# Kernel tuning notes

Hardware: AMD Instinct MI355X
Metric: run time of the kernel (lower is better)

Reference implementation:

```python
import jax, jax.numpy as jnp
import numpy as np

IMG = 640
TOPK = 13
NC = 1
ALPHA = 0.5
BETA = 6.0
EPS = 1e-9
IOU_EPS = 1e-7


def _make_anchors():
    pts = []
    for s in (8, 16, 32):
        n = IMG // s
        g = (jnp.arange(n, dtype=jnp.float32) + 0.5) * s
        yy, xx = jnp.meshgrid(g, g, indexing="ij")
        pts.append(jnp.stack([xx.ravel(), yy.ravel()], axis=-1))
    return jnp.concatenate(pts, axis=0)  # [8400, 2]


def _make_boxes(key, prefix):
    k1, k2 = jax.random.split(key)
    cxcy = jax.random.uniform(k1, prefix + (2,), minval=32.0, maxval=IMG - 32.0)
    wh = jax.random.uniform(k2, prefix + (2,), minval=8.0, maxval=128.0)
    return jnp.concatenate([cxcy - wh / 2, cxcy + wh / 2], axis=-1)


def setup_inputs() -> dict:
    key = jax.random.key(0)
    B, G, NA = 32, 64, 8400
    k1, k2, k3, k4 = jax.random.split(key, 4)
    pd_scores = jax.random.uniform(k1, (B, NA, 1))
    pd_bboxes = _make_boxes(k2, (B, NA))
    anc_points = _make_anchors()
    gt_labels = jnp.zeros((B, G, 1), dtype=jnp.int64)  # single class
    gt_bboxes = _make_boxes(k3, (B, G))
    num_gt = jax.random.randint(k4, (B, 1), 1, G + 1)
    mask_gt = (jnp.arange(G)[None, :] < num_gt).astype(jnp.float32)[..., None]
    return {
        "pd_scores": pd_scores,
        "pd_bboxes": pd_bboxes,
        "anc_points": anc_points,
        "gt_labels": gt_labels,
        "gt_bboxes": gt_bboxes,
        "mask_gt": mask_gt,
    }


def _iou_xyxy(gt, pd):
    # gt: [B,G,1,4], pd: [B,1,NA,4] -> [B,G,NA]
    ix1 = jnp.maximum(gt[..., 0], pd[..., 0])
    iy1 = jnp.maximum(gt[..., 1], pd[..., 1])
    ix2 = jnp.minimum(gt[..., 2], pd[..., 2])
    iy2 = jnp.minimum(gt[..., 3], pd[..., 3])
    inter = jnp.clip(ix2 - ix1, 0) * jnp.clip(iy2 - iy1, 0)
    a1 = (gt[..., 2] - gt[..., 0]) * (gt[..., 3] - gt[..., 1])
    a2 = (pd[..., 2] - pd[..., 0]) * (pd[..., 3] - pd[..., 1])
    return inter / (a1 + a2 - inter + IOU_EPS)


def reference(pd_scores, pd_bboxes, anc_points, gt_labels, gt_bboxes, mask_gt):
    B, G, _ = gt_bboxes.shape
    NA = pd_bboxes.shape[1]

    # candidates inside GT boxes: [B,G,NA]
    ap = anc_points[None, None]                   # [1,1,NA,2]
    gb = gt_bboxes[:, :, None]                    # [B,G,1,4]
    lt = ap - gb[..., :2]
    rb = gb[..., 2:] - ap
    mask_in_gts = (jnp.concatenate([lt, rb], axis=-1).min(axis=-1) > 0).astype(jnp.float32)
    valid_mask = mask_in_gts * mask_gt[..., 0][:, :, None]

    # pairwise IoU + alignment metric
    overlaps = jnp.clip(_iou_xyxy(gt_bboxes[:, :, None], pd_bboxes[:, None]), 0)  # [B,G,NA]
    bbox_scores = pd_scores[..., 0][:, None, :]                                   # [B,1,NA]
    align_metric = jnp.clip(bbox_scores, 0) ** ALPHA * overlaps ** BETA * valid_mask

    # top-k per GT over anchors (threshold-based mask, including ties, like torch ref)
    k = min(TOPK, NA)
    topk_vals = jax.lax.top_k(align_metric, k)[0]          # [B,G,k]
    threshold = topk_vals[..., -1:]
    mask_topk = (align_metric >= threshold).astype(jnp.float32)

    mask_pos = mask_topk * valid_mask

    # conflict resolution: anchor claimed by >1 GT -> GT with max IoU
    fg = mask_pos.sum(axis=1)                              # [B,NA]
    disputed = fg[:, None, :] > 1                          # [B,1,NA]
    best_gt = jnp.argmax(overlaps, axis=1)                 # [B,NA]
    one_hot_gt = (jnp.arange(G)[None, :, None] == best_gt[:, None, :]).astype(jnp.float32)
    mask_pos = jnp.where(disputed, one_hot_gt, mask_pos)
    fg_mask = mask_pos.sum(axis=1)                         # [B,NA]
    target_gt_idx = jnp.argmax(mask_pos, axis=1)           # [B,NA]

    # gather targets
    target_labels = jnp.clip(
        jnp.take_along_axis(gt_labels[..., 0], target_gt_idx, axis=1), 0)      # [B,NA]
    target_bboxes = jnp.take_along_axis(gt_bboxes, target_gt_idx[..., None], axis=1)  # [B,NA,4]
    target_scores = jax.nn.one_hot(target_labels, NC, dtype=jnp.float32) * fg_mask[..., None]

    # alignment normalization
    am = align_metric * mask_pos
    pos_align_max = am.max(axis=-1, keepdims=True)
    pos_iou_max = (overlaps * mask_pos).max(axis=-1, keepdims=True)
    norm_weights = (am / (pos_align_max + EPS) * pos_iou_max).max(axis=1)       # [B,NA]
    target_scores = target_scores * norm_weights[..., None]

    return target_labels, target_bboxes, target_scores, fg_mask > 0
```

## Files before the change

### kernel.cpp

```cpp
#include <hip/hip_runtime.h>

#define TOPK_K 13
#define KPAD 16


__device__ __forceinline__ float iou_clip(const float4 g, const float4 p) {
    float ix1 = fmaxf(g.x, p.x), iy1 = fmaxf(g.y, p.y);
    float ix2 = fminf(g.z, p.z), iy2 = fminf(g.w, p.w);
    float iw = fmaxf(ix2 - ix1, 0.f);
    float ih = fmaxf(iy2 - iy1, 0.f);
    float inter = iw * ih;
    float a1 = (g.z - g.x) * (g.w - g.y);
    float a2 = (p.z - p.x) * (p.w - p.y);
    float iou = inter / (a1 + a2 - inter + 1e-7f);
    return fmaxf(iou, 0.f);
}

__device__ __forceinline__ float in_box(float ax, float ay, const float4 g) {
    float m = fminf(fminf(ax - g.x, ay - g.y), fminf(g.z - ax, g.w - ay));
    return (m > 0.f) ? 1.f : 0.f;
}

__device__ __forceinline__ float align_metric_f(float sqs, float iou, float valid) {
    float p2 = iou * iou;
    float p6 = p2 * p2 * p2;
    return sqs * p6 * valid;
}

__global__ __launch_bounds__(256) void k_init(
    int* __restrict__ cnt, int* __restrict__ ming,
    int* __restrict__ pam, int* __restrict__ pim, int BNA, int BG, int G)
{
    int i = blockIdx.x * blockDim.x + threadIdx.x;
    if (i < BNA) { cnt[i] = 0; ming[i] = G; }
    if (i < BG)  { pam[i] = 0; pim[i] = 0; }
}

__global__ __launch_bounds__(256) void k_gt(
    const float* __restrict__ pd_scores, const float* __restrict__ pd_bboxes,
    const float* __restrict__ gt_bboxes, const float* __restrict__ mask_gt,
    int* __restrict__ cnt, int* __restrict__ ming,
    int B, int G, int NA)
{
    int w = blockIdx.x * (blockDim.x >> 6) + (threadIdx.x >> 6);
    int lane = threadIdx.x & 63;
    if (w >= B * G) return;
    if (mask_gt[w] == 0.f) return;
    int b = w / G;
    int g = w - b * G;
    float4 gb = *(const float4*)(gt_bboxes + (size_t)w * 4);
    const float* ps = pd_scores + (size_t)b * NA;
    const float* pb = pd_bboxes + (size_t)b * NA * 4;

    int rix0[3], riy0[3], rix1[3], riy1[3];
    #pragma unroll
    for (int lvl = 0; lvl < 3; ++lvl) {
        const int n = (lvl == 0) ? 80 : (lvl == 1 ? 40 : 20);
        const float sf = (float)(8 << lvl);
        rix0[lvl] = max(0,     (int)floorf(gb.x / sf - 0.5f));
        riy0[lvl] = max(0,     (int)floorf(gb.y / sf - 0.5f));
        rix1[lvl] = min(n - 1, (int)ceilf (gb.z / sf - 0.5f));
        riy1[lvl] = min(n - 1, (int)ceilf (gb.w / sf - 0.5f));
    }

    float t[KPAD];
    #pragma unroll
    for (int i = 0; i < KPAD; ++i) t[i] = 0.f;

    #pragma unroll
    for (int lvl = 0; lvl < 3; ++lvl) {
        const int n   = (lvl == 0) ? 80 : (lvl == 1 ? 40 : 20);
        const int off = (lvl == 0) ? 0  : (lvl == 1 ? 6400 : 8000);
        const float sf = (float)(8 << lvl);
        int wdt = rix1[lvl] - rix0[lvl] + 1, hgt = riy1[lvl] - riy0[lvl] + 1;
        if (wdt <= 0 || hgt <= 0) continue;
        int n_c = wdt * hgt;
        for (int c = lane; c < n_c; c += 64) {
            int ix = rix0[lvl] + (c % wdt);
            int iy = riy0[lvl] + (c / wdt);
            float ax = (ix + 0.5f) * sf;
            float ay = (iy + 0.5f) * sf;
            if (in_box(ax, ay, gb) != 0.f) {
                int a = off + iy * n + ix;
                float4 p = *(const float4*)(pb + (size_t)a * 4);
                float iou = iou_clip(gb, p);
                float sqs = sqrtf(fmaxf(ps[a], 0.f));
                float am = align_metric_f(sqs, iou, 1.f);
                if (am > t[KPAD - 1]) {
                    t[KPAD - 1] = am;
                    #pragma unroll
                    for (int i = KPAD - 1; i > 0; --i) {
                        float hi = fmaxf(t[i - 1], t[i]);
                        float lo = fminf(t[i - 1], t[i]);
                        t[i - 1] = hi; t[i] = lo;
                    }
                }
            }
        }
    }

    for (int off = 1; off < 64; off <<= 1) {
        float o[KPAD], m[KPAD];
        #pragma unroll
        for (int i = 0; i < KPAD; ++i) o[i] = __shfl_xor(t[i], off, 64);
        #pragma unroll
        for (int i = 0; i < KPAD; ++i) m[i] = fmaxf(t[i], o[KPAD - 1 - i]);
        #pragma unroll
        for (int s = 8; s >= 1; s >>= 1) {
            #pragma unroll
            for (int i = 0; i < KPAD; ++i) {
                if ((i & s) == 0) {
                    float hi = fmaxf(m[i], m[i + s]);
                    float lo = fminf(m[i], m[i + s]);
                    m[i] = hi; m[i + s] = lo;
                }
            }
        }
        #pragma unroll
        for (int i = 0; i < KPAD; ++i) t[i] = m[i];
    }
    float thr = t[TOPK_K - 1];

    int* cntb  = cnt  + (size_t)b * NA;
    int* mingb = ming + (size_t)b * NA;
    #pragma unroll
    for (int lvl = 0; lvl < 3; ++lvl) {
        const int n   = (lvl == 0) ? 80 : (lvl == 1 ? 40 : 20);
        const int off = (lvl == 0) ? 0  : (lvl == 1 ? 6400 : 8000);
        const float sf = (float)(8 << lvl);
        int wdt = rix1[lvl] - rix0[lvl] + 1, hgt = riy1[lvl] - riy0[lvl] + 1;
        if (wdt <= 0 || hgt <= 0) continue;
        int n_c = wdt * hgt;
        for (int c = lane; c < n_c; c += 64) {
            int ix = rix0[lvl] + (c % wdt);
            int iy = riy0[lvl] + (c / wdt);
            float ax = (ix + 0.5f) * sf;
            float ay = (iy + 0.5f) * sf;
            if (in_box(ax, ay, gb) != 0.f) {
                int a = off + iy * n + ix;
                float4 p = *(const float4*)(pb + (size_t)a * 4);
                float iou = iou_clip(gb, p);
                float sqs = sqrtf(fmaxf(ps[a], 0.f));
                float am = align_metric_f(sqs, iou, 1.f);
                if (am >= thr) {
                    atomicAdd(&cntb[a], 1);
                    atomicMin(&mingb[a], g);
                }
            }
        }
    }
}

__global__ __launch_bounds__(256) void k_anchor(
    const float* __restrict__ pd_scores, const float* __restrict__ pd_bboxes,
    const float* __restrict__ anc, const int* __restrict__ gt_labels,
    const float* __restrict__ gt_bboxes, const float* __restrict__ mask_gt,
    const int* __restrict__ cnt_arr, const int* __restrict__ ming_arr,
    float* __restrict__ out_labels, float* __restrict__ out_bboxes,
    float* __restrict__ out_fg,
    int* __restrict__ ws_tgt, float* __restrict__ ws_amv,
    int* __restrict__ pam, int* __restrict__ pim,
    int B, int G, int NA)
{
    __shared__ float4 sbox[64];
    __shared__ float smask[64];
    __shared__ int   slab[64];

    int b = blockIdx.y;
    int tid = threadIdx.x;
    if (tid < G) {
        sbox[tid]  = *(const float4*)(gt_bboxes + ((size_t)b * G + tid) * 4);
        smask[tid] = mask_gt[b * G + tid];
        slab[tid]  = gt_labels[b * G + tid];
    }
    __syncthreads();

    int a = blockIdx.x * blockDim.x + tid;
    bool active = (a < NA);
    int lane = tid & 63;
    size_t o = (size_t)b * NA + (size_t)(active ? a : 0);

    int cntv = 0;
    float4 p = make_float4(0.f, 0.f, 0.f, 0.f);
    if (active) {
        cntv = cnt_arr[o];
        p = *(const float4*)(pd_bboxes + o * 4);
    }

    int tgt = 0;
    float fgm = (cntv != 0) ? 1.f : 0.f;
    if (cntv == 1) tgt = ming_arr[o];

    unsigned long long dm = __ballot(cntv > 1);
    while (dm) {
        int l = __ffsll((long long)dm) - 1;
        dm &= dm - 1;
        float4 pl;
        pl.x = __shfl(p.x, l, 64); pl.y = __shfl(p.y, l, 64);
        pl.z = __shfl(p.z, l, 64); pl.w = __shfl(p.w, l, 64);
        float iou = (lane < G) ? iou_clip(sbox[lane], pl) : -1.f;
        int g = lane;
        #pragma unroll
        for (int off = 32; off >= 1; off >>= 1) {
            float oi = __shfl_xor(iou, off, 64);
            int   og = __shfl_xor(g,   off, 64);
            if (oi > iou || (oi == iou && og < g)) { iou = oi; g = og; }
        }
        if (lane == l) tgt = g;
    }

    if (!active) return;

    float4 gbt = sbox[tgt];
    float ax = anc[2 * a], ay = anc[2 * a + 1];
    float sqs = sqrtf(fmaxf(pd_scores[o], 0.f));
    float vt = in_box(ax, ay, gbt) * smask[tgt];
    float iout = iou_clip(gbt, p);
    float amt = align_metric_f(sqs, iout, vt);
    float amv = (fgm != 0.f) ? amt : 0.f;
    float iov = (fgm != 0.f) ? iout : 0.f;

    int lbl = slab[tgt]; if (lbl < 0) lbl = 0;
    out_labels[o] = (float)lbl;
    *(float4*)(out_bboxes + o * 4) = gbt;
    out_fg[o] = fgm;
    ws_tgt[o] = tgt;
    ws_amv[o] = amv;

    if (fgm != 0.f) {
        int gi = b * G + tgt;
        atomicMax(&pam[gi], __float_as_int(amv));
        atomicMax(&pim[gi], __float_as_int(iov));
    }
}

__global__ __launch_bounds__(256) void k_scores(
    const int* __restrict__ ws_tgt, const float* __restrict__ ws_amv,
    const int* __restrict__ pam, const int* __restrict__ pim,
    const float* __restrict__ out_labels,
    float* __restrict__ out_scores,
    int B, int G, int NA)
{
    int i = blockIdx.x * blockDim.x + threadIdx.x;
    if (i >= B * NA) return;
    int b = i / NA;
    int tgt = ws_tgt[i];
    float amv = ws_amv[i];
    float pa = __int_as_float(pam[b * G + tgt]);
    float pi = __int_as_float(pim[b * G + tgt]);
    float wgt = amv / (pa + 1e-9f) * pi;
    float onehot = (out_labels[i] == 0.f) ? 1.f : 0.f;
    out_scores[i] = onehot * wgt;
}

extern "C" void kernel_launch(void* const* d_in, const int* in_sizes, int n_in,
                              void* d_out, int out_size, void* d_ws, size_t ws_size,
                              hipStream_t stream) {
    const float* pd_scores = (const float*)d_in[0];
    const float* pd_bboxes = (const float*)d_in[1];
    const float* anc       = (const float*)d_in[2];
    const int*   gt_labels = (const int*)d_in[3];
    const float* gt_bboxes = (const float*)d_in[4];
    const float* mask_gt   = (const float*)d_in[5];

    int NA = in_sizes[2] / 2;
    int B  = in_sizes[0] / NA;
    int G  = in_sizes[4] / (B * 4);

    float* out = (float*)d_out;
    float* out_labels = out;
    float* out_bboxes = out_labels + (size_t)B * NA;
    float* out_scores = out_bboxes + (size_t)B * NA * 4;
    float* out_fg     = out_scores + (size_t)B * NA;

    int BG = B * G;
    int BNA = B * NA;
    int* cnt      = (int*)d_ws;
    int* ming     = cnt + BNA;
    int* pam      = ming + BNA;
    int* pim      = pam + BG;
    int* ws_tgt   = pim + BG;
    float* ws_amv = (float*)(ws_tgt + BNA);

    k_init<<<dim3((BNA + 255) / 256), dim3(256), 0, stream>>>(
        cnt, ming, pam, pim, BNA, BG, G);

    k_gt<<<dim3((BG + 3) / 4), dim3(256), 0, stream>>>(
        pd_scores, pd_bboxes, gt_bboxes, mask_gt, cnt, ming, B, G, NA);

    k_anchor<<<dim3((NA + 255) / 256, B), dim3(256), 0, stream>>>(
        pd_scores, pd_bboxes, anc, gt_labels, gt_bboxes, mask_gt, cnt, ming,
        out_labels, out_bboxes, out_fg, ws_tgt, ws_amv, pam, pim, B, G, NA);

    k_scores<<<dim3((BNA + 255) / 256), dim3(256), 0, stream>>>(
        ws_tgt, ws_amv, pam, pim, out_labels, out_scores, B, G, NA);
}
```

Measured before the change: 49.26 us.

## Replace global atomics with per-GT claim lists and fuse anchor stages per batch

The per-GT kernel now compacts its positive anchors into a per-GT list in workspace instead of doing global atomicAdd/atomicMin. A single per-batch kernel with 1024 threads builds the claim counts and minimum GT index in shared memory, resolves disputed anchors, and computes the per-GT max reductions with shared atomics. It then writes the normalized scores itself, which removes the init, anchor and score kernels and their global workspace round trips. The trade-off is that only 32 blocks run, leaving most of the GPU idle. It also relies on hardcoded caps (416 claims per GT, NA 8400, G at most 64).

```diff
diff --git a/kernel.cpp b/kernel.cpp
--- a/kernel.cpp
+++ b/kernel.cpp
@@ -2,6 +2,9 @@
 
 #define TOPK_K 13
 #define KPAD 16
+#define CAP 416
+#define NA_C 8400
+#define RTHREADS 1024
 
 
 __device__ __forceinline__ float iou_clip(const float4 g, const float4 p) {
@@ -27,27 +30,28 @@
     return sqs * p6 * valid;
 }
 
-__global__ __launch_bounds__(256) void k_init(
-    int* __restrict__ cnt, int* __restrict__ ming,
-    int* __restrict__ pam, int* __restrict__ pim, int BNA, int BG, int G)
-{
-    int i = blockIdx.x * blockDim.x + threadIdx.x;
-    if (i < BNA) { cnt[i] = 0; ming[i] = G; }
-    if (i < BG)  { pam[i] = 0; pim[i] = 0; }
+__device__ __forceinline__ void anc_xy(int i, float& ax, float& ay) {
+    int lvl = (i < 6400) ? 0 : (i < 8000 ? 1 : 2);
+    int n   = (lvl == 0) ? 80 : (lvl == 1 ? 40 : 20);
+    int off = (lvl == 0) ? 0  : (lvl == 1 ? 6400 : 8000);
+    float sf = (float)(8 << lvl);
+    int r = i - off;
+    int iy = r / n, ix = r - iy * n;
+    ax = (ix + 0.5f) * sf;
+    ay = (iy + 0.5f) * sf;
 }
 
 __global__ __launch_bounds__(256) void k_gt(
     const float* __restrict__ pd_scores, const float* __restrict__ pd_bboxes,
     const float* __restrict__ gt_bboxes, const float* __restrict__ mask_gt,
-    int* __restrict__ cnt, int* __restrict__ ming,
+    int* __restrict__ claims, int* __restrict__ nclaim,
     int B, int G, int NA)
 {
     int w = blockIdx.x * (blockDim.x >> 6) + (threadIdx.x >> 6);
     int lane = threadIdx.x & 63;
     if (w >= B * G) return;
-    if (mask_gt[w] == 0.f) return;
+    if (mask_gt[w] == 0.f) { if (lane == 0) nclaim[w] = 0; return; }
     int b = w / G;
-    int g = w - b * G;
     float4 gb = *(const float4*)(gt_bboxes + (size_t)w * 4);
     const float* ps = pd_scores + (size_t)b * NA;
     const float* pb = pd_bboxes + (size_t)b * NA * 4;
@@ -121,8 +125,8 @@
     }
     float thr = t[TOPK_K - 1];
 
-    int* cntb  = cnt  + (size_t)b * NA;
-    int* mingb = ming + (size_t)b * NA;
+    int* listw = claims + (size_t)w * CAP;
+    int base = 0;
     #pragma unroll
     for (int lvl = 0; lvl < 3; ++lvl) {
         const int n   = (lvl == 0) ? 80 : (lvl == 1 ? 40 : 20);
@@ -131,126 +135,155 @@
         int wdt = rix1[lvl] - rix0[lvl] + 1, hgt = riy1[lvl] - riy0[lvl] + 1;
         if (wdt <= 0 || hgt <= 0) continue;
         int n_c = wdt * hgt;
-        for (int c = lane; c < n_c; c += 64) {
-            int ix = rix0[lvl] + (c % wdt);
-            int iy = riy0[lvl] + (c / wdt);
-            float ax = (ix + 0.5f) * sf;
-            float ay = (iy + 0.5f) * sf;
-            if (in_box(ax, ay, gb) != 0.f) {
-                int a = off + iy * n + ix;
-                float4 p = *(const float4*)(pb + (size_t)a * 4);
-                float iou = iou_clip(gb, p);
-                float sqs = sqrtf(fmaxf(ps[a], 0.f));
-                float am = align_metric_f(sqs, iou, 1.f);
-                if (am >= thr) {
-                    atomicAdd(&cntb[a], 1);
-                    atomicMin(&mingb[a], g);
+        for (int c0 = 0; c0 < n_c; c0 += 64) {
+            int c = c0 + lane;
+            bool pass = false;
+            int a = 0;
+            if (c < n_c) {
+                int ix = rix0[lvl] + (c % wdt);
+                int iy = riy0[lvl] + (c / wdt);
+                float ax = (ix + 0.5f) * sf;
+                float ay = (iy + 0.5f) * sf;
+                if (in_box(ax, ay, gb) != 0.f) {
+                    a = off + iy * n + ix;
+                    float4 p = *(const float4*)(pb + (size_t)a * 4);
+                    float iou = iou_clip(gb, p);
+                    float sqs = sqrtf(fmaxf(ps[a], 0.f));
+                    float am = align_metric_f(sqs, iou, 1.f);
+                    pass = (am >= thr);
                 }
             }
-        }
-    }
-}
-
-__global__ __launch_bounds__(256) void k_anchor(
+            unsigned long long bal = __ballot(pass);
+            if (pass) {
+                int idx = base + (int)__popcll(bal & ((1ull << lane) - 1ull));
+                listw[idx] = a;
+            }
+            base += (int)__popcll(bal);
+        }
+    }
+    if (lane == 0) nclaim[w] = base;
+}
+
+__global__ __launch_bounds__(RTHREADS) void k_rest(
     const float* __restrict__ pd_scores, const float* __restrict__ pd_bboxes,
-    const float* __restrict__ anc, const int* __restrict__ gt_labels,
-    const float* __restrict__ gt_bboxes, const float* __restrict__ mask_gt,
-    const int* __restrict__ cnt_arr, const int* __restrict__ ming_arr,
+    const int* __restrict__ gt_labels, const float* __restrict__ gt_bboxes,
+    const float* __restrict__ mask_gt,
+    const int* __restrict__ claims, const int* __restrict__ nclaim,
     float* __restrict__ out_labels, float* __restrict__ out_bboxes,
-    float* __restrict__ out_fg,
-    int* __restrict__ ws_tgt, float* __restrict__ ws_amv,
-    int* __restrict__ pam, int* __restrict__ pim,
-    int B, int G, int NA)
+    float* __restrict__ out_scores, float* __restrict__ out_fg,
+    int G, int NA)
 {
+    __shared__ int    sclaim[NA_C];
     __shared__ float4 sbox[64];
-    __shared__ float smask[64];
-    __shared__ int   slab[64];
-
-    int b = blockIdx.y;
-    int tid = threadIdx.x;
-    if (tid < G) {
+    __shared__ float  smask[64];
+    __shared__ int    slab[64];
+    __shared__ int    spam[64];
+    __shared__ int    spim[64];
+
+    const int b   = blockIdx.x;
+    const int tid = threadIdx.x;
+    const int lane = tid & 63;
+
+    for (int i = tid; i < NA; i += RTHREADS) sclaim[i] = 0;
+    if (tid < 64) {
         sbox[tid]  = *(const float4*)(gt_bboxes + ((size_t)b * G + tid) * 4);
         smask[tid] = mask_gt[b * G + tid];
-        slab[tid]  = gt_labels[b * G + tid];
+        int l = gt_labels[b * G + tid];
+        slab[tid]  = (l < 0) ? 0 : l;
+        spam[tid]  = 0;
+        spim[tid]  = 0;
     }
     __syncthreads();
 
-    int a = blockIdx.x * blockDim.x + tid;
-    bool active = (a < NA);
-    int lane = tid & 63;
-    size_t o = (size_t)b * NA + (size_t)(active ? a : 0);
-
-    int cntv = 0;
-    float4 p = make_float4(0.f, 0.f, 0.f, 0.f);
-    if (active) {
-        cntv = cnt_arr[o];
-        p = *(const float4*)(pd_bboxes + o * 4);
-    }
-
-    int tgt = 0;
-    float fgm = (cntv != 0) ? 1.f : 0.f;
-    if (cntv == 1) tgt = ming_arr[o];
-
-    unsigned long long dm = __ballot(cntv > 1);
-    while (dm) {
-        int l = __ffsll((long long)dm) - 1;
-        dm &= dm - 1;
-        float4 pl;
-        pl.x = __shfl(p.x, l, 64); pl.y = __shfl(p.y, l, 64);
-        pl.z = __shfl(p.z, l, 64); pl.w = __shfl(p.w, l, 64);
-        float iou = (lane < G) ? iou_clip(sbox[lane], pl) : -1.f;
-        int g = lane;
-        #pragma unroll
-        for (int off = 32; off >= 1; off >>= 1) {
-            float oi = __shfl_xor(iou, off, 64);
-            int   og = __shfl_xor(g,   off, 64);
-            if (oi > iou || (oi == iou && og < g)) { iou = oi; g = og; }
-        }
-        if (lane == l) tgt = g;
-    }
-
-    if (!active) return;
-
-    float4 gbt = sbox[tgt];
-    float ax = anc[2 * a], ay = anc[2 * a + 1];
-    float sqs = sqrtf(fmaxf(pd_scores[o], 0.f));
-    float vt = in_box(ax, ay, gbt) * smask[tgt];
-    float iout = iou_clip(gbt, p);
-    float amt = align_metric_f(sqs, iout, vt);
-    float amv = (fgm != 0.f) ? amt : 0.f;
-    float iov = (fgm != 0.f) ? iout : 0.f;
-
-    int lbl = slab[tgt]; if (lbl < 0) lbl = 0;
-    out_labels[o] = (float)lbl;
-    *(float4*)(out_bboxes + o * 4) = gbt;
-    out_fg[o] = fgm;
-    ws_tgt[o] = tgt;
-    ws_amv[o] = amv;
-
-    if (fgm != 0.f) {
-        int gi = b * G + tgt;
-        atomicMax(&pam[gi], __float_as_int(amv));
-        atomicMax(&pim[gi], __float_as_int(iov));
-    }
-}
-
-__global__ __launch_bounds__(256) void k_scores(
-    const int* __restrict__ ws_tgt, const float* __restrict__ ws_amv,
-    const int* __restrict__ pam, const int* __restrict__ pim,
-    const float* __restrict__ out_labels,
-    float* __restrict__ out_scores,
-    int B, int G, int NA)
-{
-    int i = blockIdx.x * blockDim.x + threadIdx.x;
-    if (i >= B * NA) return;
-    int b = i / NA;
-    int tgt = ws_tgt[i];
-    float amv = ws_amv[i];
-    float pa = __int_as_float(pam[b * G + tgt]);
-    float pi = __int_as_float(pim[b * G + tgt]);
-    float wgt = amv / (pa + 1e-9f) * pi;
-    float onehot = (out_labels[i] == 0.f) ? 1.f : 0.f;
-    out_scores[i] = onehot * wgt;
+    {
+        int wid = tid >> 6;
+        for (int g = wid; g < G; g += (RTHREADS >> 6)) {
+            int w = b * G + g;
+            int len = nclaim[w];
+            const int* lw = claims + (size_t)w * CAP;
+            int add = (1 << 20) + g;
+            for (int j = lane; j < len; j += 64)
+                atomicAdd(&sclaim[lw[j]], add);
+        }
+    }
+    __syncthreads();
+
+    const float4 gl = sbox[lane];
+    const float* ps = pd_scores + (size_t)b * NA;
+    const float* pb = pd_bboxes + (size_t)b * NA * 4;
+
+    for (int i0 = 0; i0 < NA; i0 += RTHREADS) {
+        int i = i0 + tid;
+        bool act = (i < NA);
+        int v = act ? sclaim[i] : 0;
+        int c = v >> 20;
+        float4 p = act ? *(const float4*)(pb + (size_t)i * 4)
+                       : make_float4(0.f, 0.f, 0.f, 0.f);
+
+        int tgt = (c == 1) ? (v & 0xFFFFF) : 0;
+
+        unsigned long long dm = __ballot(c > 1);
+        while (dm) {
+            int l = __ffsll((long long)dm) - 1;
+            dm &= dm - 1;
+            float4 pl;
+            pl.x = __shfl(p.x, l, 64); pl.y = __shfl(p.y, l, 64);
+            pl.z = __shfl(p.z, l, 64); pl.w = __shfl(p.w, l, 64);
+            float iou = iou_clip(gl, pl);
+            int g = lane;
+            #pragma unroll
+            for (int off = 32; off >= 1; off >>= 1) {
+                float oi = __shfl_xor(iou, off, 64);
+                int   og = __shfl_xor(g,   off, 64);
+                if (oi > iou || (oi == iou && og < g)) { iou = oi; g = og; }
+            }
+            if (lane == l) tgt = g;
+        }
+
+        if (act) {
+            float4 gbt = sbox[tgt];
+            float ax, ay; anc_xy(i, ax, ay);
+            float sqs = sqrtf(fmaxf(ps[i], 0.f));
+            float vt  = in_box(ax, ay, gbt) * smask[tgt];
+            float iout = iou_clip(gbt, p);
+            float amt = align_metric_f(sqs, iout, vt);
+            bool fg = (c != 0);
+            float amv = fg ? amt : 0.f;
+            float iov = fg ? iout : 0.f;
+
+            size_t o = (size_t)b * NA + i;
+            out_labels[o] = (float)slab[tgt];
+            *(float4*)(out_bboxes + o * 4) = gbt;
+            out_fg[o] = fg ? 1.f : 0.f;
+            sclaim[i] = tgt | (fg ? 256 : 0);
+            if (fg) {
+                atomicMax(&spam[tgt], __float_as_int(amv));
+                atomicMax(&spim[tgt], __float_as_int(iov));
+            }
+        }
+    }
+    __syncthreads();
+
+    for (int i = tid; i < NA; i += RTHREADS) {
+        int v = sclaim[i];
+        int tgt = v & 63;
+        bool fg = (v & 256) != 0;
+        float amv = 0.f;
+        if (fg) {
+            float4 gbt = sbox[tgt];
+            float4 p = *(const float4*)(pb + (size_t)i * 4);
+            float ax, ay; anc_xy(i, ax, ay);
+            float sqs = sqrtf(fmaxf(ps[i], 0.f));
+            float vt  = in_box(ax, ay, gbt) * smask[tgt];
+            float iout = iou_clip(gbt, p);
+            amv = align_metric_f(sqs, iout, vt);
+        }
+        float pa = __int_as_float(spam[tgt]);
+        float pi = __int_as_float(spim[tgt]);
+        float wgt = amv / (pa + 1e-9f) * pi;
+        float onehot = (slab[tgt] == 0) ? 1.f : 0.f;
+        out_scores[(size_t)b * NA + i] = onehot * wgt;
+    }
 }
 
 extern "C" void kernel_launch(void* const* d_in, const int* in_sizes, int n_in,
@@ -258,7 +291,6 @@
                               hipStream_t stream) {
     const float* pd_scores = (const float*)d_in[0];
     const float* pd_bboxes = (const float*)d_in[1];
-    const float* anc       = (const float*)d_in[2];
     const int*   gt_labels = (const int*)d_in[3];
     const float* gt_bboxes = (const float*)d_in[4];
     const float* mask_gt   = (const float*)d_in[5];
@@ -274,24 +306,13 @@
     float* out_fg     = out_scores + (size_t)B * NA;
 
     int BG = B * G;
-    int BNA = B * NA;
-    int* cnt      = (int*)d_ws;
-    int* ming     = cnt + BNA;
-    int* pam      = ming + BNA;
-    int* pim      = pam + BG;
-    int* ws_tgt   = pim + BG;
-    float* ws_amv = (float*)(ws_tgt + BNA);
-
-    k_init<<<dim3((BNA + 255) / 256), dim3(256), 0, stream>>>(
-        cnt, ming, pam, pim, BNA, BG, G);
+    int* claims = (int*)d_ws;
+    int* nclaim = claims + (size_t)BG * CAP;
 
     k_gt<<<dim3((BG + 3) / 4), dim3(256), 0, stream>>>(
-        pd_scores, pd_bboxes, gt_bboxes, mask_gt, cnt, ming, B, G, NA);
-
-    k_anchor<<<dim3((NA + 255) / 256, B), dim3(256), 0, stream>>>(
-        pd_scores, pd_bboxes, anc, gt_labels, gt_bboxes, mask_gt, cnt, ming,
-        out_labels, out_bboxes, out_fg, ws_tgt, ws_amv, pam, pim, B, G, NA);
-
-    k_scores<<<dim3((BNA + 255) / 256), dim3(256), 0, stream>>>(
-        ws_tgt, ws_amv, pam, pim, out_labels, out_scores, B, G, NA);
-}
+        pd_scores, pd_bboxes, gt_bboxes, mask_gt, claims, nclaim, B, G, NA);
+
+    k_rest<<<dim3(B), dim3(RTHREADS), 0, stream>>>(
+        pd_scores, pd_bboxes, gt_labels, gt_bboxes, mask_gt, claims, nclaim,
+        out_labels, out_bboxes, out_scores, out_fg, G, NA);
+}
```

After: 97.63 us. +98.2%, slower.
